# Kernel tuning notes

Measured on AMD Instinct MI355X. Metric: run time of the kernel, lower is better.

The kernel has to match this reference:

```python
import jax, jax.numpy as jnp
import numpy as np

B, N, T = 32, 128, 16          # batch, nb_nodes, total algorithm steps (1 no-hint + T-1 hinted)
FN, FE, FG, FH = 16, 8, 8, 16  # raw node/edge/graph/hint feature widths
H, DEC = 128, 64               # hidden_dim, decoder output width
MSG_STEPS = 3                  # msg_passing_steps
NEG = -1e9


def setup_inputs() -> dict:
    key = jax.random.key(0)
    ks = jax.random.split(key, 20)
    def nrm(k, shape, s=0.1):
        return jax.random.normal(k, shape, dtype=jnp.float32) * s
    return dict(
        node_inputs=nrm(ks[0], (B, N, FN), 1.0),
        edge_inputs=nrm(ks[1], (B, N, N, FE), 1.0),
        graph_inputs=nrm(ks[2], (B, FG), 1.0),
        hints_in=nrm(ks[3], (T - 1, B, N, FH), 1.0),
        adj=jax.random.randint(ks[4], (B, N, N), 0, 2).astype(jnp.int32),
        W_enc_n=nrm(ks[5], (FN, H)),
        W_enc_h=nrm(ks[6], (FH, H)),
        W_enc_e=nrm(ks[7], (FE, H)),
        W_enc_g=nrm(ks[8], (FG, H)),
        W_m1=nrm(ks[9], (2 * H, H)),
        W_m2=nrm(ks[10], (2 * H, H)),
        W_me=nrm(ks[11], (H, H)),
        W_mg=nrm(ks[12], (H, H)),
        W_o1=nrm(ks[13], (2 * H, H)),
        W_o2=nrm(ks[14], (H, H)),
        W_dec_n=nrm(ks[15], (H, DEC)),
        W_dec_e=nrm(ks[16], (H, DEC)),
    )


def reference(node_inputs, edge_inputs, graph_inputs, hints_in, adj,
              W_enc_n, W_enc_h, W_enc_e, W_enc_g,
              W_m1, W_m2, W_me, W_mg, W_o1, W_o2, W_dec_n, W_dec_e):
    adj_m = (adj > 0)[..., None]                      # [B,N,N,1] receiver i <- sender j
    # Encoder (edge/graph parts are step-invariant; hoisting is math-equivalent)
    edge_fts = edge_inputs @ W_enc_e                  # [B,N,N,H]
    graph_fts = graph_inputs @ W_enc_g                # [B,H]
    msg_e = edge_fts @ W_me                           # [B,N,N,H]
    msg_g = (graph_fts @ W_mg)[:, None, None, :]      # [B,1,1,H]
    base_node = node_inputs @ W_enc_n                 # [B,N,H]
    # Step 0 has no hint; steps 1..T-1 use hints_in[step-1]
    hints_all = jnp.concatenate(
        [jnp.zeros((1,) + hints_in.shape[1:], hints_in.dtype), hints_in], axis=0)

    def step(hidden, hint):
        node_fts = base_node + hint @ W_enc_h         # [B,N,H]
        edge_out = None
        for _ in range(MSG_STEPS):                    # PGN message passing
            z = jnp.concatenate([node_fts, hidden], axis=-1)   # [B,N,2H]
            msgs = jax.nn.relu((z @ W_m1)[:, :, None, :]
                               + (z @ W_m2)[:, None, :, :]
                               + msg_e + msg_g)       # [B,N,N,H]
            agg = jnp.where(adj_m, msgs, NEG).max(axis=2)      # max over senders j
            hidden = jax.nn.relu(z @ W_o1 + agg @ W_o2)        # [B,N,H]
            edge_out = msgs
        # Decoder: node head + masked-max-pooled edge head
        edge_agg = jnp.where(adj_m, edge_out, NEG).max(axis=2)
        out = hidden @ W_dec_n + edge_agg @ W_dec_e   # [B,N,DEC]
        return hidden, out

    hidden0 = jnp.zeros((node_inputs.shape[0], node_inputs.shape[1], H),
                        node_inputs.dtype)
    _, outs = jax.lax.scan(step, hidden0, hints_all)  # outs: [T,B,N,DEC]
    return outs
```

## Files before the change

kernel.cpp:

```cpp
#include <hip/hip_runtime.h>
#include <hip/hip_bf16.h>
#include <stdint.h>

#define BB 32
#define NN 128
#define TT 16
#define FN 16
#define FE 8
#define FG 8
#define FH 16
#define HH 128
#define DEC 64


__global__ __launch_bounds__(HH) void prep1(const float* __restrict__ node,
                                            const float* __restrict__ Wn,
                                            float* __restrict__ base_node,
                                            float* __restrict__ hid) {
    int row = blockIdx.x;
    int h = threadIdx.x;
    float acc = 0.f;
#pragma unroll
    for (int f = 0; f < FN; ++f)
        acc += node[row * FN + f] * Wn[f * HH + h];
    base_node[row * HH + h] = acc;
    hid[row * HH + h] = 0.f;
}

__global__ __launch_bounds__(HH) void prep2(const float* __restrict__ graph,
                                            const float* __restrict__ Wg,
                                            const float* __restrict__ Wmg,
                                            const float* __restrict__ Wee,
                                            const float* __restrict__ Wme,
                                            float* __restrict__ mg,
                                            float* __restrict__ We) {
    int h = threadIdx.x;
    if (blockIdx.x < BB) {
        int b = blockIdx.x;
        __shared__ float gf[HH];
        float acc = 0.f;
#pragma unroll
        for (int f = 0; f < FG; ++f) acc += graph[b * FG + f] * Wg[f * HH + h];
        gf[h] = acc;
        __syncthreads();
        float a2 = 0.f;
#pragma unroll 16
        for (int k = 0; k < HH; ++k) a2 += gf[k] * Wmg[k * HH + h];
        mg[b * HH + h] = a2;
    } else {
        int f = blockIdx.x - BB;
        float acc = 0.f;
#pragma unroll 16
        for (int k = 0; k < HH; ++k) acc += Wee[f * HH + k] * Wme[k * HH + h];
        We[f * HH + h] = acc;
    }
}

__device__ __forceinline__ uint32_t bf16rne(float v) {
    uint32_t b = __float_as_uint(v);
    return (b + 0x7fffu + ((b >> 16) & 1u)) >> 16;
}

__global__ __launch_bounds__(HH) void prep3(const float* __restrict__ edge,
                                            const int* __restrict__ adj,
                                            uint4* __restrict__ eg16,
                                            int* __restrict__ jl,
                                            int* __restrict__ cnt) {
    int bi = blockIdx.x;
    int j = threadIdx.x;
    __shared__ int w0cnt, totc, j0s;
    bool valid = adj[(size_t)bi * NN + j] > 0;
    unsigned long long mask = __ballot(valid);
    int lane = j & 63;
    int wave = j >> 6;
    int prefix = __popcll(mask & ((1ull << lane) - 1ull));
    int wcount = __popcll(mask);
    if (wave == 0 && lane == 0) w0cnt = wcount;
    __syncthreads();
    int base = (wave == 1) ? w0cnt : 0;
    if (wave == 1 && lane == 0) totc = w0cnt + wcount;
    int pos = base + prefix;
    if (valid && pos == 0) j0s = j;
    __syncthreads();
    int c = totc;
    int cpad = (c + 7) & ~7;
    if (j == 0) cnt[bi] = cpad;

    if (valid) {
        jl[bi * NN + pos] = j;
        const float* src = edge + ((size_t)bi * NN + j) * FE;
        uint4 r;
        r.x = bf16rne(src[0]) | (bf16rne(src[1]) << 16);
        r.y = bf16rne(src[2]) | (bf16rne(src[3]) << 16);
        r.z = bf16rne(src[4]) | (bf16rne(src[5]) << 16);
        r.w = bf16rne(src[6]) | (bf16rne(src[7]) << 16);
        eg16[(size_t)bi * NN + pos] = r;
    }
    if (c > 0 && j >= c && j < cpad) {
        int j0 = j0s;
        jl[bi * NN + j] = j0;
        const float* src = edge + ((size_t)bi * NN + j0) * FE;
        uint4 r;
        r.x = bf16rne(src[0]) | (bf16rne(src[1]) << 16);
        r.y = bf16rne(src[2]) | (bf16rne(src[3]) << 16);
        r.z = bf16rne(src[4]) | (bf16rne(src[5]) << 16);
        r.w = bf16rne(src[6]) | (bf16rne(src[7]) << 16);
        eg16[(size_t)bi * NN + j] = r;
    }
}

__global__ __launch_bounds__(256) void k0_nf(
    const float* __restrict__ base_node, const float* __restrict__ hints,
    const float* __restrict__ Wh,
    const float* __restrict__ Wm1, const float* __restrict__ Wm2,
    const float* __restrict__ Wo1, const float* __restrict__ mg,
    float* __restrict__ zpart) {
    __shared__ float zs[8][HH];
    const int lane = threadIdx.x & 127;
    const int half = threadIdx.x >> 7;
    const int bid = blockIdx.x;
    const int t = bid >> 9;
    const int bl = bid & 511;
    const int tile = (bl & 7) * 64 + (bl >> 3);
    const int row0 = tile * 8;

#pragma unroll
    for (int r = 0; r < 4; ++r) {
        int rr = half * 4 + r;
        int row = row0 + rr;
        float nf = base_node[row * HH + lane];
        if (t > 0) {
            const float* hr = hints + ((size_t)(t - 1) * BB * NN + row) * FH;
#pragma unroll
            for (int f = 0; f < FH; ++f) nf = fmaf(hr[f], Wh[f * HH + lane], nf);
        }
        zs[rr][lane] = nf;
    }
    __syncthreads();

    float acc[4][3];
#pragma unroll
    for (int r = 0; r < 4; ++r) { acc[r][0] = 0.f; acc[r][1] = 0.f; acc[r][2] = 0.f; }
    const int h4 = half * 4;

#pragma unroll 4
    for (int kk = 0; kk < 32; ++kk) {
        const int k0 = kk * 4;
        float4 z0 = *(const float4*)&zs[h4 + 0][k0];
        float4 z1 = *(const float4*)&zs[h4 + 1][k0];
        float4 z2 = *(const float4*)&zs[h4 + 2][k0];
        float4 z3 = *(const float4*)&zs[h4 + 3][k0];
#define K0U(COMP, KO)                                                   \
        {                                                               \
            const float w1 = Wm1[(k0 + KO) * HH + lane];                \
            const float w2 = Wm2[(k0 + KO) * HH + lane];                \
            const float w3 = Wo1[(k0 + KO) * HH + lane];                \
            acc[0][0] = fmaf(z0.COMP, w1, acc[0][0]);                   \
            acc[1][0] = fmaf(z1.COMP, w1, acc[1][0]);                   \
            acc[2][0] = fmaf(z2.COMP, w1, acc[2][0]);                   \
            acc[3][0] = fmaf(z3.COMP, w1, acc[3][0]);                   \
            acc[0][1] = fmaf(z0.COMP, w2, acc[0][1]);                   \
            acc[1][1] = fmaf(z1.COMP, w2, acc[1][1]);                   \
            acc[2][1] = fmaf(z2.COMP, w2, acc[2][1]);                   \
            acc[3][1] = fmaf(z3.COMP, w2, acc[3][1]);                   \
            acc[0][2] = fmaf(z0.COMP, w3, acc[0][2]);                   \
            acc[1][2] = fmaf(z1.COMP, w3, acc[1][2]);                   \
            acc[2][2] = fmaf(z2.COMP, w3, acc[2][2]);                   \
            acc[3][2] = fmaf(z3.COMP, w3, acc[3][2]);                   \
        }
        K0U(x, 0) K0U(y, 1) K0U(z, 2) K0U(w, 3)
#undef K0U
    }

    const int b = row0 >> 7;
    const float mgv = mg[b * HH + lane];
#pragma unroll
    for (int r = 0; r < 4; ++r) {
        const int row = row0 + h4 + r;
        const size_t o = ((size_t)t * 3 * 4096) * HH;
        zpart[o + ((size_t)0 * 4096 + row) * HH + lane] = acc[r][0] + mgv;
        zpart[o + ((size_t)1 * 4096 + row) * HH + lane] = acc[r][1];
        zpart[o + ((size_t)2 * 4096 + row) * HH + lane] = acc[r][2];
    }
}

__global__ __launch_bounds__(256) void k1_gemm(
    const float* __restrict__ hid,
    const float* __restrict__ Wm1, const float* __restrict__ Wm2,
    const float* __restrict__ Wo1, const float* __restrict__ zpart,
    float* __restrict__ m1p, float* __restrict__ m2, float* __restrict__ o1,
    int t) {
    __shared__ float zs[8][HH];
    const int lane = threadIdx.x & 127;
    const int half = threadIdx.x >> 7;
    const int bid = blockIdx.x;
    const int tile = (bid & 7) * 64 + (bid >> 3);
    const int row0 = tile * 8;

#pragma unroll
    for (int r = 0; r < 4; ++r) {
        int rr = half * 4 + r;
        zs[rr][lane] = hid[(row0 + rr) * HH + lane];
    }
    __syncthreads();

    float acc[4][3];
#pragma unroll
    for (int r = 0; r < 4; ++r) { acc[r][0] = 0.f; acc[r][1] = 0.f; acc[r][2] = 0.f; }
    const int h4 = half * 4;
    const float* __restrict__ W1 = Wm1 + HH * HH;
    const float* __restrict__ W2 = Wm2 + HH * HH;
    const float* __restrict__ W3 = Wo1 + HH * HH;

#pragma unroll 4
    for (int kk = 0; kk < 32; ++kk) {
        const int k0 = kk * 4;
        float4 z0 = *(const float4*)&zs[h4 + 0][k0];
        float4 z1 = *(const float4*)&zs[h4 + 1][k0];
        float4 z2 = *(const float4*)&zs[h4 + 2][k0];
        float4 z3 = *(const float4*)&zs[h4 + 3][k0];
#define K1U(COMP, KO)                                                   \
        {                                                               \
            const float w1 = W1[(k0 + KO) * HH + lane];                 \
            const float w2 = W2[(k0 + KO) * HH + lane];                 \
            const float w3 = W3[(k0 + KO) * HH + lane];                 \
            acc[0][0] = fmaf(z0.COMP, w1, acc[0][0]);                   \
            acc[1][0] = fmaf(z1.COMP, w1, acc[1][0]);                   \
            acc[2][0] = fmaf(z2.COMP, w1, acc[2][0]);                   \
            acc[3][0] = fmaf(z3.COMP, w1, acc[3][0]);                   \
            acc[0][1] = fmaf(z0.COMP, w2, acc[0][1]);                   \
            acc[1][1] = fmaf(z1.COMP, w2, acc[1][1]);                   \
            acc[2][1] = fmaf(z2.COMP, w2, acc[2][1]);                   \
            acc[3][1] = fmaf(z3.COMP, w2, acc[3][1]);                   \
            acc[0][2] = fmaf(z0.COMP, w3, acc[0][2]);                   \
            acc[1][2] = fmaf(z1.COMP, w3, acc[1][2]);                   \
            acc[2][2] = fmaf(z2.COMP, w3, acc[2][2]);                   \
            acc[3][2] = fmaf(z3.COMP, w3, acc[3][2]);                   \
        }
        K1U(x, 0) K1U(y, 1) K1U(z, 2) K1U(w, 3)
#undef K1U
    }

    const size_t zo = ((size_t)t * 3 * 4096) * HH;
#pragma unroll
    for (int r = 0; r < 4; ++r) {
        const int row = row0 + h4 + r;
        m1p[row * HH + lane] = acc[r][0] + zpart[zo + ((size_t)0 * 4096 + row) * HH + lane];
        m2[row * HH + lane]  = acc[r][1] + zpart[zo + ((size_t)1 * 4096 + row) * HH + lane];
        o1[row * HH + lane]  = acc[r][2] + zpart[zo + ((size_t)2 * 4096 + row) * HH + lane];
    }
}

__global__ __launch_bounds__(HH) void k2_max(
    const uint4* __restrict__ eg16, const int* __restrict__ jl,
    const int* __restrict__ cnt, const float* __restrict__ We,
    const float* __restrict__ m1p, const float* __restrict__ m2,
    const float* __restrict__ o1, const float* __restrict__ Wo2,
    const float* __restrict__ Wdn, const float* __restrict__ Wde,
    float* __restrict__ hid, float* __restrict__ out, int t, int last) {
    __shared__ float agg_lds[HH];
    __shared__ float hnew_lds[HH];
    const int h = threadIdx.x;
    const int bid = blockIdx.x;
    const int bi = (bid & 7) * 512 + (bid >> 3);
    const int b = bi >> 7;

    const float we0 = We[0 * HH + h], we1 = We[1 * HH + h];
    const float we2 = We[2 * HH + h], we3 = We[3 * HH + h];
    const float we4 = We[4 * HH + h], we5 = We[5 * HH + h];
    const float we6 = We[6 * HH + h], we7 = We[7 * HH + h];

    const uint4* __restrict__ egp = eg16 + (size_t)bi * NN;
    const int* __restrict__ jlb = jl + bi * NN;
    const float* __restrict__ m2b = m2 + (size_t)b * NN * HH;
    const int cp = cnt[bi];
    const float m1v = m1p[bi * HH + h];
    const float o1v = o1[bi * HH + h];

    float M = -3e38f;
    const int nch = cp >> 3;
    for (int ch = 0; ch < nch; ++ch) {
        const int k0 = ch * 8;
        uint4 raw[8];
        int jj[8];
        float mv[8];
#pragma unroll
        for (int s = 0; s < 8; ++s) raw[s] = egp[k0 + s];
#pragma unroll
        for (int s = 0; s < 8; ++s) jj[s] = jlb[k0 + s];
#pragma unroll
        for (int s = 0; s < 8; ++s) mv[s] = m2b[jj[s] * HH + h];
#pragma unroll
        for (int s = 0; s < 8; ++s) {
            uint32_t x = raw[s].x, y = raw[s].y, z = raw[s].z, w = raw[s].w;
            float e = __uint_as_float(x << 16) * we0;
            e = fmaf(__uint_as_float(x & 0xffff0000u), we1, e);
            e = fmaf(__uint_as_float(y << 16), we2, e);
            e = fmaf(__uint_as_float(y & 0xffff0000u), we3, e);
            e = fmaf(__uint_as_float(z << 16), we4, e);
            e = fmaf(__uint_as_float(z & 0xffff0000u), we5, e);
            e = fmaf(__uint_as_float(w << 16), we6, e);
            e = fmaf(__uint_as_float(w & 0xffff0000u), we7, e);
            M = fmaxf(M, e + mv[s]);
        }
    }
    float agg = (cp > 0) ? fmaxf(m1v + M, 0.f) : -1e9f;
    agg_lds[h] = agg;
    __syncthreads();

    float acc = o1v;
    const float4* a4 = (const float4*)agg_lds;
#pragma unroll 8
    for (int kk = 0; kk < 32; ++kk) {
        float4 a = a4[kk];
        acc = fmaf(a.x, Wo2[(kk * 4 + 0) * HH + h], acc);
        acc = fmaf(a.y, Wo2[(kk * 4 + 1) * HH + h], acc);
        acc = fmaf(a.z, Wo2[(kk * 4 + 2) * HH + h], acc);
        acc = fmaf(a.w, Wo2[(kk * 4 + 3) * HH + h], acc);
    }
    float hv = fmaxf(acc, 0.f);
    hid[bi * HH + h] = hv;

    if (last) {
        hnew_lds[h] = hv;
        __syncthreads();
        if (h < DEC) {
            float a = 0.f, e2 = 0.f;
            const float4* h4p = (const float4*)hnew_lds;
#pragma unroll 8
            for (int kk = 0; kk < 32; ++kk) {
                float4 hv4 = h4p[kk];
                float4 av4 = a4[kk];
                a = fmaf(hv4.x, Wdn[(kk * 4 + 0) * DEC + h], a);
                a = fmaf(hv4.y, Wdn[(kk * 4 + 1) * DEC + h], a);
                a = fmaf(hv4.z, Wdn[(kk * 4 + 2) * DEC + h], a);
                a = fmaf(hv4.w, Wdn[(kk * 4 + 3) * DEC + h], a);
                e2 = fmaf(av4.x, Wde[(kk * 4 + 0) * DEC + h], e2);
                e2 = fmaf(av4.y, Wde[(kk * 4 + 1) * DEC + h], e2);
                e2 = fmaf(av4.z, Wde[(kk * 4 + 2) * DEC + h], e2);
                e2 = fmaf(av4.w, Wde[(kk * 4 + 3) * DEC + h], e2);
            }
            out[(((size_t)t * BB + b) * NN + (bi & 127)) * DEC + h] = a + e2;
        }
    }
}

extern "C" void kernel_launch(void* const* d_in, const int* in_sizes, int n_in,
                              void* d_out, int out_size, void* d_ws, size_t ws_size,
                              hipStream_t stream) {
    const float* node = (const float*)d_in[0];
    const float* edge = (const float*)d_in[1];
    const float* graph = (const float*)d_in[2];
    const float* hints = (const float*)d_in[3];
    const int* adj = (const int*)d_in[4];
    const float* Wn = (const float*)d_in[5];
    const float* Wh = (const float*)d_in[6];
    const float* Wee = (const float*)d_in[7];
    const float* Wg = (const float*)d_in[8];
    const float* Wm1 = (const float*)d_in[9];
    const float* Wm2 = (const float*)d_in[10];
    const float* Wme = (const float*)d_in[11];
    const float* Wmg = (const float*)d_in[12];
    const float* Wo1 = (const float*)d_in[13];
    const float* Wo2 = (const float*)d_in[14];
    const float* Wdn = (const float*)d_in[15];
    const float* Wde = (const float*)d_in[16];

    float* ws = (float*)d_ws;
    float* base_node = ws;
    float* We = ws + 524288;
    float* mg = ws + 525312;
    float* m1p = ws + 529408;
    float* m2 = ws + 1053696;
    float* o1 = ws + 1577984;
    float* hid = ws + 2102272;
    uint4* eg16 = (uint4*)(ws + 2626560);
    int* jl = (int*)(ws + 4723712);
    int* cnt = (int*)(ws + 5248000);
    float* zpart = ws + 5252096;
    float* out = (float*)d_out;

    prep1<<<BB * NN, HH, 0, stream>>>(node, Wn, base_node, hid);
    prep2<<<BB + FE, HH, 0, stream>>>(graph, Wg, Wmg, Wee, Wme, mg, We);
    prep3<<<BB * NN, HH, 0, stream>>>(edge, adj, eg16, jl, cnt);
    k0_nf<<<8192, 256, 0, stream>>>(base_node, hints, Wh, Wm1, Wm2, Wo1, mg,
                                    zpart);

    for (int t = 0; t < TT; ++t) {
        for (int ms = 0; ms < 3; ++ms) {
            k1_gemm<<<512, 256, 0, stream>>>(hid, Wm1, Wm2, Wo1, zpart,
                                             m1p, m2, o1, t);
            k2_max<<<BB * NN, HH, 0, stream>>>(eg16, jl, cnt, We, m1p, m2, o1,
                                               Wo2, Wdn, Wde, hid, out, t,
                                               ms == 2 ? 1 : 0);
        }
    }
}
```

Measured before the change: 2.058 ms.

## Fuse message max-aggregation with next-iteration GEMM into a single kernel

Merges the separate GEMM and max-aggregation kernels into one 1024-thread kernel per 8-row tile. Each launch stages the batch's m2 projection into LDS, computes the masked max, the Wo2 update and optionally the decoder, then immediately computes the next iteration's m1/m2/o1 from the new hidden state in LDS. Outputs go to ping-pong buffers, so launches drop from 96 to 48 and the hidden-state round trip through global memory disappears. The cost is 64KB+ of LDS per block, which limits occupancy, and only 256 of 1024 threads do the next-step GEMM.

```diff
diff --git a/kernel.cpp b/kernel.cpp
--- a/kernel.cpp
+++ b/kernel.cpp
@@ -15,8 +15,7 @@
 
 __global__ __launch_bounds__(HH) void prep1(const float* __restrict__ node,
                                             const float* __restrict__ Wn,
-                                            float* __restrict__ base_node,
-                                            float* __restrict__ hid) {
+                                            float* __restrict__ base_node) {
     int row = blockIdx.x;
     int h = threadIdx.x;
     float acc = 0.f;
@@ -24,7 +23,6 @@
     for (int f = 0; f < FN; ++f)
         acc += node[row * FN + f] * Wn[f * HH + h];
     base_node[row * HH + h] = acc;
-    hid[row * HH + h] = 0.f;
 }
 
 __global__ __launch_bounds__(HH) void prep2(const float* __restrict__ graph,
@@ -184,114 +182,64 @@
     }
 }
 
-__global__ __launch_bounds__(256) void k1_gemm(
-    const float* __restrict__ hid,
+__global__ __launch_bounds__(1024, 8) void k12(
+    const uint4* __restrict__ eg16, const int* __restrict__ jl,
+    const int* __restrict__ cnt, const float* __restrict__ We,
+    const float* __restrict__ m1c, const float* __restrict__ m2c,
+    const float* __restrict__ o1c,
     const float* __restrict__ Wm1, const float* __restrict__ Wm2,
-    const float* __restrict__ Wo1, const float* __restrict__ zpart,
-    float* __restrict__ m1p, float* __restrict__ m2, float* __restrict__ o1,
-    int t) {
-    __shared__ float zs[8][HH];
-    const int lane = threadIdx.x & 127;
-    const int half = threadIdx.x >> 7;
+    const float* __restrict__ Wo1, const float* __restrict__ Wo2,
+    const float* __restrict__ Wdn, const float* __restrict__ Wde,
+    const float* __restrict__ zp,
+    float* __restrict__ m1n, float* __restrict__ m2n, float* __restrict__ o1n,
+    float* __restrict__ out, int t, int last, int do_next) {
+    __shared__ float m2_lds[NN][HH];
+    __shared__ float agg_lds[8][HH];
+    __shared__ float hv_lds[8][HH];
+    const int tid = threadIdx.x;
     const int bid = blockIdx.x;
     const int tile = (bid & 7) * 64 + (bid >> 3);
-    const int row0 = tile * 8;
-
-#pragma unroll
-    for (int r = 0; r < 4; ++r) {
-        int rr = half * 4 + r;
-        zs[rr][lane] = hid[(row0 + rr) * HH + lane];
-    }
-    __syncthreads();
-
-    float acc[4][3];
-#pragma unroll
-    for (int r = 0; r < 4; ++r) { acc[r][0] = 0.f; acc[r][1] = 0.f; acc[r][2] = 0.f; }
-    const int h4 = half * 4;
-    const float* __restrict__ W1 = Wm1 + HH * HH;
-    const float* __restrict__ W2 = Wm2 + HH * HH;
-    const float* __restrict__ W3 = Wo1 + HH * HH;
-
-#pragma unroll 4
-    for (int kk = 0; kk < 32; ++kk) {
-        const int k0 = kk * 4;
-        float4 z0 = *(const float4*)&zs[h4 + 0][k0];
-        float4 z1 = *(const float4*)&zs[h4 + 1][k0];
-        float4 z2 = *(const float4*)&zs[h4 + 2][k0];
-        float4 z3 = *(const float4*)&zs[h4 + 3][k0];
-#define K1U(COMP, KO)                                                   \
-        {                                                               \
-            const float w1 = W1[(k0 + KO) * HH + lane];                 \
-            const float w2 = W2[(k0 + KO) * HH + lane];                 \
-            const float w3 = W3[(k0 + KO) * HH + lane];                 \
-            acc[0][0] = fmaf(z0.COMP, w1, acc[0][0]);                   \
-            acc[1][0] = fmaf(z1.COMP, w1, acc[1][0]);                   \
-            acc[2][0] = fmaf(z2.COMP, w1, acc[2][0]);                   \
-            acc[3][0] = fmaf(z3.COMP, w1, acc[3][0]);                   \
-            acc[0][1] = fmaf(z0.COMP, w2, acc[0][1]);                   \
-            acc[1][1] = fmaf(z1.COMP, w2, acc[1][1]);                   \
-            acc[2][1] = fmaf(z2.COMP, w2, acc[2][1]);                   \
-            acc[3][1] = fmaf(z3.COMP, w2, acc[3][1]);                   \
-            acc[0][2] = fmaf(z0.COMP, w3, acc[0][2]);                   \
-            acc[1][2] = fmaf(z1.COMP, w3, acc[1][2]);                   \
-            acc[2][2] = fmaf(z2.COMP, w3, acc[2][2]);                   \
-            acc[3][2] = fmaf(z3.COMP, w3, acc[3][2]);                   \
-        }
-        K1U(x, 0) K1U(y, 1) K1U(z, 2) K1U(w, 3)
-#undef K1U
-    }
-
-    const size_t zo = ((size_t)t * 3 * 4096) * HH;
-#pragma unroll
-    for (int r = 0; r < 4; ++r) {
-        const int row = row0 + h4 + r;
-        m1p[row * HH + lane] = acc[r][0] + zpart[zo + ((size_t)0 * 4096 + row) * HH + lane];
-        m2[row * HH + lane]  = acc[r][1] + zpart[zo + ((size_t)1 * 4096 + row) * HH + lane];
-        o1[row * HH + lane]  = acc[r][2] + zpart[zo + ((size_t)2 * 4096 + row) * HH + lane];
-    }
-}
-
-__global__ __launch_bounds__(HH) void k2_max(
-    const uint4* __restrict__ eg16, const int* __restrict__ jl,
-    const int* __restrict__ cnt, const float* __restrict__ We,
-    const float* __restrict__ m1p, const float* __restrict__ m2,
-    const float* __restrict__ o1, const float* __restrict__ Wo2,
-    const float* __restrict__ Wdn, const float* __restrict__ Wde,
-    float* __restrict__ hid, float* __restrict__ out, int t, int last) {
-    __shared__ float agg_lds[HH];
-    __shared__ float hnew_lds[HH];
-    const int h = threadIdx.x;
-    const int bid = blockIdx.x;
-    const int bi = (bid & 7) * 512 + (bid >> 3);
-    const int b = bi >> 7;
+    const int b = tile >> 4;
+    const int ig = tile & 15;
+    const int bi0 = b * NN + ig * 8;
+
+    {
+        const float4* src = (const float4*)(m2c + (size_t)b * NN * HH);
+        float4* dst = (float4*)&m2_lds[0][0];
+#pragma unroll
+        for (int u = 0; u < 4; ++u) dst[u * 1024 + tid] = src[u * 1024 + tid];
+    }
+
+    const int il = tid >> 7;
+    const int h = tid & 127;
+    const int bi = bi0 + il;
 
     const float we0 = We[0 * HH + h], we1 = We[1 * HH + h];
     const float we2 = We[2 * HH + h], we3 = We[3 * HH + h];
     const float we4 = We[4 * HH + h], we5 = We[5 * HH + h];
     const float we6 = We[6 * HH + h], we7 = We[7 * HH + h];
-
+    const int cp = cnt[bi];
+    const float m1v = m1c[bi * HH + h];
+    const float o1v = o1c[bi * HH + h];
     const uint4* __restrict__ egp = eg16 + (size_t)bi * NN;
     const int* __restrict__ jlb = jl + bi * NN;
-    const float* __restrict__ m2b = m2 + (size_t)b * NN * HH;
-    const int cp = cnt[bi];
-    const float m1v = m1p[bi * HH + h];
-    const float o1v = o1[bi * HH + h];
+    __syncthreads();
 
     float M = -3e38f;
-    const int nch = cp >> 3;
+    const int nch = cp >> 2;
     for (int ch = 0; ch < nch; ++ch) {
-        const int k0 = ch * 8;
-        uint4 raw[8];
-        int jj[8];
-        float mv[8];
-#pragma unroll
-        for (int s = 0; s < 8; ++s) raw[s] = egp[k0 + s];
-#pragma unroll
-        for (int s = 0; s < 8; ++s) jj[s] = jlb[k0 + s];
-#pragma unroll
-        for (int s = 0; s < 8; ++s) mv[s] = m2b[jj[s] * HH + h];
-#pragma unroll
-        for (int s = 0; s < 8; ++s) {
+        const int k0 = ch * 4;
+        uint4 raw[4];
+        int jj[4];
+        float mv[4];
+#pragma unroll
+        for (int s = 0; s < 4; ++s) raw[s] = egp[k0 + s];
+#pragma unroll
+        for (int s = 0; s < 4; ++s) jj[s] = jlb[k0 + s];
+#pragma unroll
+        for (int s = 0; s < 4; ++s) mv[s] = m2_lds[jj[s]][h];
+#pragma unroll
+        for (int s = 0; s < 4; ++s) {
             uint32_t x = raw[s].x, y = raw[s].y, z = raw[s].z, w = raw[s].w;
             float e = __uint_as_float(x << 16) * we0;
             e = fmaf(__uint_as_float(x & 0xffff0000u), we1, e);
@@ -305,11 +253,11 @@
         }
     }
     float agg = (cp > 0) ? fmaxf(m1v + M, 0.f) : -1e9f;
-    agg_lds[h] = agg;
+    agg_lds[il][h] = agg;
     __syncthreads();
 
     float acc = o1v;
-    const float4* a4 = (const float4*)agg_lds;
+    const float4* a4 = (const float4*)&agg_lds[il][0];
 #pragma unroll 8
     for (int kk = 0; kk < 32; ++kk) {
         float4 a = a4[kk];
@@ -318,29 +266,81 @@
         acc = fmaf(a.z, Wo2[(kk * 4 + 2) * HH + h], acc);
         acc = fmaf(a.w, Wo2[(kk * 4 + 3) * HH + h], acc);
     }
-    float hv = fmaxf(acc, 0.f);
-    hid[bi * HH + h] = hv;
-
-    if (last) {
-        hnew_lds[h] = hv;
-        __syncthreads();
-        if (h < DEC) {
-            float a = 0.f, e2 = 0.f;
-            const float4* h4p = (const float4*)hnew_lds;
+    hv_lds[il][h] = fmaxf(acc, 0.f);
+    __syncthreads();
+
+    if (last && tid >= 512) {
+        const int dl = (tid - 512) >> 6;
+        const int hh = (tid - 512) & 63;
+        float a = 0.f, e2 = 0.f;
+        const float4* h4p = (const float4*)&hv_lds[dl][0];
+        const float4* ag4 = (const float4*)&agg_lds[dl][0];
 #pragma unroll 8
-            for (int kk = 0; kk < 32; ++kk) {
-                float4 hv4 = h4p[kk];
-                float4 av4 = a4[kk];
-                a = fmaf(hv4.x, Wdn[(kk * 4 + 0) * DEC + h], a);
-                a = fmaf(hv4.y, Wdn[(kk * 4 + 1) * DEC + h], a);
-                a = fmaf(hv4.z, Wdn[(kk * 4 + 2) * DEC + h], a);
-                a = fmaf(hv4.w, Wdn[(kk * 4 + 3) * DEC + h], a);
-                e2 = fmaf(av4.x, Wde[(kk * 4 + 0) * DEC + h], e2);
-                e2 = fmaf(av4.y, Wde[(kk * 4 + 1) * DEC + h], e2);
-                e2 = fmaf(av4.z, Wde[(kk * 4 + 2) * DEC + h], e2);
-                e2 = fmaf(av4.w, Wde[(kk * 4 + 3) * DEC + h], e2);
+        for (int kk = 0; kk < 32; ++kk) {
+            float4 hv4 = h4p[kk];
+            float4 av4 = ag4[kk];
+            a = fmaf(hv4.x, Wdn[(kk * 4 + 0) * DEC + hh], a);
+            a = fmaf(hv4.y, Wdn[(kk * 4 + 1) * DEC + hh], a);
+            a = fmaf(hv4.z, Wdn[(kk * 4 + 2) * DEC + hh], a);
+            a = fmaf(hv4.w, Wdn[(kk * 4 + 3) * DEC + hh], a);
+            e2 = fmaf(av4.x, Wde[(kk * 4 + 0) * DEC + hh], e2);
+            e2 = fmaf(av4.y, Wde[(kk * 4 + 1) * DEC + hh], e2);
+            e2 = fmaf(av4.z, Wde[(kk * 4 + 2) * DEC + hh], e2);
+            e2 = fmaf(av4.w, Wde[(kk * 4 + 3) * DEC + hh], e2);
+        }
+        out[(((size_t)t * BB + b) * NN + ig * 8 + dl) * DEC + hh] = a + e2;
+    }
+
+    if (do_next && tid < 256) {
+        const int lane = tid & 127;
+        const int half = tid >> 7;
+        const int h4 = half * 4;
+        const float* __restrict__ W1 = Wm1 + HH * HH;
+        const float* __restrict__ W2 = Wm2 + HH * HH;
+        const float* __restrict__ W3 = Wo1 + HH * HH;
+
+        float acc2[4][3];
+#pragma unroll
+        for (int r = 0; r < 4; ++r) {
+            acc2[r][0] = 0.f; acc2[r][1] = 0.f; acc2[r][2] = 0.f;
+        }
+#pragma unroll 4
+        for (int kk = 0; kk < 32; ++kk) {
+            const int k0 = kk * 4;
+            float4 z0 = *(const float4*)&hv_lds[h4 + 0][k0];
+            float4 z1 = *(const float4*)&hv_lds[h4 + 1][k0];
+            float4 z2 = *(const float4*)&hv_lds[h4 + 2][k0];
+            float4 z3 = *(const float4*)&hv_lds[h4 + 3][k0];
+#define K1U(COMP, KO)                                                   \
+            {                                                           \
+                const float w1 = W1[(k0 + KO) * HH + lane];             \
+                const float w2 = W2[(k0 + KO) * HH + lane];             \
+                const float w3 = W3[(k0 + KO) * HH + lane];             \
+                acc2[0][0] = fmaf(z0.COMP, w1, acc2[0][0]);             \
+                acc2[1][0] = fmaf(z1.COMP, w1, acc2[1][0]);             \
+                acc2[2][0] = fmaf(z2.COMP, w1, acc2[2][0]);             \
+                acc2[3][0] = fmaf(z3.COMP, w1, acc2[3][0]);             \
+                acc2[0][1] = fmaf(z0.COMP, w2, acc2[0][1]);             \
+                acc2[1][1] = fmaf(z1.COMP, w2, acc2[1][1]);             \
+                acc2[2][1] = fmaf(z2.COMP, w2, acc2[2][1]);             \
+                acc2[3][1] = fmaf(z3.COMP, w2, acc2[3][1]);             \
+                acc2[0][2] = fmaf(z0.COMP, w3, acc2[0][2]);             \
+                acc2[1][2] = fmaf(z1.COMP, w3, acc2[1][2]);             \
+                acc2[2][2] = fmaf(z2.COMP, w3, acc2[2][2]);             \
+                acc2[3][2] = fmaf(z3.COMP, w3, acc2[3][2]);             \
             }
-            out[(((size_t)t * BB + b) * NN + (bi & 127)) * DEC + h] = a + e2;
+            K1U(x, 0) K1U(y, 1) K1U(z, 2) K1U(w, 3)
+#undef K1U
+        }
+#pragma unroll
+        for (int r = 0; r < 4; ++r) {
+            const int row = bi0 + h4 + r;
+            m1n[(size_t)row * HH + lane] =
+                acc2[r][0] + zp[((size_t)0 * 4096 + row) * HH + lane];
+            m2n[(size_t)row * HH + lane] =
+                acc2[r][1] + zp[((size_t)1 * 4096 + row) * HH + lane];
+            o1n[(size_t)row * HH + lane] =
+                acc2[r][2] + zp[((size_t)2 * 4096 + row) * HH + lane];
         }
     }
 }
@@ -370,29 +370,46 @@
     float* base_node = ws;
     float* We = ws + 524288;
     float* mg = ws + 525312;
-    float* m1p = ws + 529408;
-    float* m2 = ws + 1053696;
-    float* o1 = ws + 1577984;
-    float* hid = ws + 2102272;
-    uint4* eg16 = (uint4*)(ws + 2626560);
-    int* jl = (int*)(ws + 4723712);
-    int* cnt = (int*)(ws + 5248000);
-    float* zpart = ws + 5252096;
+    uint4* eg16 = (uint4*)(ws + 529408);
+    int* jl = (int*)(ws + 2626560);
+    int* cnt = (int*)(ws + 3150848);
+    float* zpart = ws + 3154944;
+    float* bufA = ws + 28320768;
+    float* bufB = ws + 29893632;
     float* out = (float*)d_out;
 
-    prep1<<<BB * NN, HH, 0, stream>>>(node, Wn, base_node, hid);
+    const size_t MS = (size_t)4096 * HH;
+
+    prep1<<<BB * NN, HH, 0, stream>>>(node, Wn, base_node);
     prep2<<<BB + FE, HH, 0, stream>>>(graph, Wg, Wmg, Wee, Wme, mg, We);
     prep3<<<BB * NN, HH, 0, stream>>>(edge, adj, eg16, jl, cnt);
     k0_nf<<<8192, 256, 0, stream>>>(base_node, hints, Wh, Wm1, Wm2, Wo1, mg,
                                     zpart);
 
-    for (int t = 0; t < TT; ++t) {
-        for (int ms = 0; ms < 3; ++ms) {
-            k1_gemm<<<512, 256, 0, stream>>>(hid, Wm1, Wm2, Wo1, zpart,
-                                             m1p, m2, o1, t);
-            k2_max<<<BB * NN, HH, 0, stream>>>(eg16, jl, cnt, We, m1p, m2, o1,
-                                               Wo2, Wdn, Wde, hid, out, t,
-                                               ms == 2 ? 1 : 0);
-        }
-    }
-}
+    for (int r = 0; r < 48; ++r) {
+        const int t = r / 3;
+        const int ms = r % 3;
+        const int last = (ms == 2) ? 1 : 0;
+        const int tn = t + last;
+        const int do_next = (r < 47) ? 1 : 0;
+
+        const float *m1c, *m2c, *o1c;
+        if (r == 0) {
+            m1c = zpart;
+            m2c = zpart + MS;
+            o1c = zpart + 2 * MS;
+        } else {
+            float* cb = ((r - 1) & 1) ? bufB : bufA;
+            m1c = cb; m2c = cb + MS; o1c = cb + 2 * MS;
+        }
+        float* nb = (r & 1) ? bufB : bufA;
+        float* m1n = nb;
+        float* m2n = nb + MS;
+        float* o1n = nb + 2 * MS;
+        const float* zp = zpart + (size_t)(do_next ? tn : 0) * 3 * MS;
+
+        k12<<<512, 1024, 0, stream>>>(eg16, jl, cnt, We, m1c, m2c, o1c,
+                                      Wm1, Wm2, Wo1, Wo2, Wdn, Wde, zp,
+                                      m1n, m2n, o1n, out, t, last, do_next);
+    }
+}
```

Result: slower. 2.521 ms (+22.5%).

## Fold hint encoder into precomputed weights, skip first hidden GEMM, widen k1 blocks

Applied to the files above, without the earlier changes.

Precomputes Wh·W for the three first-half weight slices and a base_node·W term once, so each k1_gemm adds the hint contribution through a 16-wide FMA instead of reading a 16-step precomputed zpart buffer. The first message step (hidden is zero) skips k1_gemm and feeds baseW straight to k2_max, and prep1 no longer zeroes hid. k1 blocks go from 256 to 512 threads with 2 rows per thread group to raise occupancy. This trades a large per-timestep zpart workspace and its writes for slightly more arithmetic inside k1.

```diff
diff --git a/kernel.cpp b/kernel.cpp
--- a/kernel.cpp
+++ b/kernel.cpp
@@ -15,8 +15,7 @@
 
 __global__ __launch_bounds__(HH) void prep1(const float* __restrict__ node,
                                             const float* __restrict__ Wn,
-                                            float* __restrict__ base_node,
-                                            float* __restrict__ hid) {
+                                            float* __restrict__ base_node) {
     int row = blockIdx.x;
     int h = threadIdx.x;
     float acc = 0.f;
@@ -24,7 +23,6 @@
     for (int f = 0; f < FN; ++f)
         acc += node[row * FN + f] * Wn[f * HH + h];
     base_node[row * HH + h] = acc;
-    hid[row * HH + h] = 0.f;
 }
 
 __global__ __launch_bounds__(HH) void prep2(const float* __restrict__ graph,
@@ -109,116 +107,107 @@
     }
 }
 
-__global__ __launch_bounds__(256) void k0_nf(
-    const float* __restrict__ base_node, const float* __restrict__ hints,
-    const float* __restrict__ Wh,
+__global__ __launch_bounds__(HH) void prepW(
+    const float* __restrict__ Wh, const float* __restrict__ Wm1,
+    const float* __restrict__ Wm2, const float* __restrict__ Wo1,
+    float* __restrict__ WhW) {
+    const int h = threadIdx.x;
+    const int m = blockIdx.x >> 4;
+    const int f = blockIdx.x & 15;
+    const float* __restrict__ W = (m == 0) ? Wm1 : (m == 1) ? Wm2 : Wo1;
+    float acc = 0.f;
+#pragma unroll 16
+    for (int k = 0; k < HH; ++k)
+        acc = fmaf(Wh[f * HH + k], W[k * HH + h], acc);
+    WhW[(m * FH + f) * HH + h] = acc;
+}
+
+__global__ __launch_bounds__(512, 4) void prepB(
+    const float* __restrict__ base_node,
     const float* __restrict__ Wm1, const float* __restrict__ Wm2,
     const float* __restrict__ Wo1, const float* __restrict__ mg,
-    float* __restrict__ zpart) {
+    float* __restrict__ baseW) {
     __shared__ float zs[8][HH];
-    const int lane = threadIdx.x & 127;
-    const int half = threadIdx.x >> 7;
+    const int tid = threadIdx.x;
+    const int lane = tid & 127;
+    const int grp = tid >> 7;
     const int bid = blockIdx.x;
-    const int t = bid >> 9;
-    const int bl = bid & 511;
-    const int tile = (bl & 7) * 64 + (bl >> 3);
+    const int tile = (bid & 7) * 64 + (bid >> 3);
     const int row0 = tile * 8;
-
-#pragma unroll
-    for (int r = 0; r < 4; ++r) {
-        int rr = half * 4 + r;
-        int row = row0 + rr;
-        float nf = base_node[row * HH + lane];
-        if (t > 0) {
-            const float* hr = hints + ((size_t)(t - 1) * BB * NN + row) * FH;
-#pragma unroll
-            for (int f = 0; f < FH; ++f) nf = fmaf(hr[f], Wh[f * HH + lane], nf);
-        }
-        zs[rr][lane] = nf;
-    }
+    const int rg0 = grp * 2, rg1 = rg0 + 1;
+
+    zs[rg0][lane] = base_node[(size_t)(row0 + rg0) * HH + lane];
+    zs[rg1][lane] = base_node[(size_t)(row0 + rg1) * HH + lane];
     __syncthreads();
 
-    float acc[4][3];
-#pragma unroll
-    for (int r = 0; r < 4; ++r) { acc[r][0] = 0.f; acc[r][1] = 0.f; acc[r][2] = 0.f; }
-    const int h4 = half * 4;
+    float acc[2][3];
+#pragma unroll
+    for (int e = 0; e < 2; ++e) { acc[e][0] = 0.f; acc[e][1] = 0.f; acc[e][2] = 0.f; }
 
 #pragma unroll 4
     for (int kk = 0; kk < 32; ++kk) {
         const int k0 = kk * 4;
-        float4 z0 = *(const float4*)&zs[h4 + 0][k0];
-        float4 z1 = *(const float4*)&zs[h4 + 1][k0];
-        float4 z2 = *(const float4*)&zs[h4 + 2][k0];
-        float4 z3 = *(const float4*)&zs[h4 + 3][k0];
-#define K0U(COMP, KO)                                                   \
+        float4 z0 = *(const float4*)&zs[rg0][k0];
+        float4 z1 = *(const float4*)&zs[rg1][k0];
+#define PBU(COMP, KO)                                                   \
         {                                                               \
             const float w1 = Wm1[(k0 + KO) * HH + lane];                \
             const float w2 = Wm2[(k0 + KO) * HH + lane];                \
             const float w3 = Wo1[(k0 + KO) * HH + lane];                \
             acc[0][0] = fmaf(z0.COMP, w1, acc[0][0]);                   \
             acc[1][0] = fmaf(z1.COMP, w1, acc[1][0]);                   \
-            acc[2][0] = fmaf(z2.COMP, w1, acc[2][0]);                   \
-            acc[3][0] = fmaf(z3.COMP, w1, acc[3][0]);                   \
             acc[0][1] = fmaf(z0.COMP, w2, acc[0][1]);                   \
             acc[1][1] = fmaf(z1.COMP, w2, acc[1][1]);                   \
-            acc[2][1] = fmaf(z2.COMP, w2, acc[2][1]);                   \
-            acc[3][1] = fmaf(z3.COMP, w2, acc[3][1]);                   \
             acc[0][2] = fmaf(z0.COMP, w3, acc[0][2]);                   \
             acc[1][2] = fmaf(z1.COMP, w3, acc[1][2]);                   \
-            acc[2][2] = fmaf(z2.COMP, w3, acc[2][2]);                   \
-            acc[3][2] = fmaf(z3.COMP, w3, acc[3][2]);                   \
-        }
-        K0U(x, 0) K0U(y, 1) K0U(z, 2) K0U(w, 3)
-#undef K0U
-    }
-
-    const int b = row0 >> 7;
-    const float mgv = mg[b * HH + lane];
-#pragma unroll
-    for (int r = 0; r < 4; ++r) {
-        const int row = row0 + h4 + r;
-        const size_t o = ((size_t)t * 3 * 4096) * HH;
-        zpart[o + ((size_t)0 * 4096 + row) * HH + lane] = acc[r][0] + mgv;
-        zpart[o + ((size_t)1 * 4096 + row) * HH + lane] = acc[r][1];
-        zpart[o + ((size_t)2 * 4096 + row) * HH + lane] = acc[r][2];
-    }
-}
-
-__global__ __launch_bounds__(256) void k1_gemm(
+        }
+        PBU(x, 0) PBU(y, 1) PBU(z, 2) PBU(w, 3)
+#undef PBU
+    }
+
+#pragma unroll
+    for (int e = 0; e < 2; ++e) {
+        const int row = row0 + grp * 2 + e;
+        const float mgv = mg[(row >> 7) * HH + lane];
+        baseW[((size_t)0 * 4096 + row) * HH + lane] = acc[e][0] + mgv;
+        baseW[((size_t)1 * 4096 + row) * HH + lane] = acc[e][1];
+        baseW[((size_t)2 * 4096 + row) * HH + lane] = acc[e][2];
+    }
+}
+
+__global__ __launch_bounds__(512, 4) void k1_gemm(
     const float* __restrict__ hid,
     const float* __restrict__ Wm1, const float* __restrict__ Wm2,
-    const float* __restrict__ Wo1, const float* __restrict__ zpart,
-    float* __restrict__ m1p, float* __restrict__ m2, float* __restrict__ o1,
+    const float* __restrict__ Wo1, const float* __restrict__ baseW,
+    const float* __restrict__ WhW, const float* __restrict__ hints,
+    float* __restrict__ m1n, float* __restrict__ m2n, float* __restrict__ o1n,
     int t) {
     __shared__ float zs[8][HH];
-    const int lane = threadIdx.x & 127;
-    const int half = threadIdx.x >> 7;
+    const int tid = threadIdx.x;
+    const int lane = tid & 127;
+    const int grp = tid >> 7;
     const int bid = blockIdx.x;
     const int tile = (bid & 7) * 64 + (bid >> 3);
     const int row0 = tile * 8;
-
-#pragma unroll
-    for (int r = 0; r < 4; ++r) {
-        int rr = half * 4 + r;
-        zs[rr][lane] = hid[(row0 + rr) * HH + lane];
-    }
+    const int rg0 = grp * 2, rg1 = rg0 + 1;
+
+    zs[rg0][lane] = hid[(size_t)(row0 + rg0) * HH + lane];
+    zs[rg1][lane] = hid[(size_t)(row0 + rg1) * HH + lane];
     __syncthreads();
 
-    float acc[4][3];
-#pragma unroll
-    for (int r = 0; r < 4; ++r) { acc[r][0] = 0.f; acc[r][1] = 0.f; acc[r][2] = 0.f; }
-    const int h4 = half * 4;
     const float* __restrict__ W1 = Wm1 + HH * HH;
     const float* __restrict__ W2 = Wm2 + HH * HH;
     const float* __restrict__ W3 = Wo1 + HH * HH;
 
+    float acc[2][3];
+#pragma unroll
+    for (int e = 0; e < 2; ++e) { acc[e][0] = 0.f; acc[e][1] = 0.f; acc[e][2] = 0.f; }
+
 #pragma unroll 4
     for (int kk = 0; kk < 32; ++kk) {
         const int k0 = kk * 4;
-        float4 z0 = *(const float4*)&zs[h4 + 0][k0];
-        float4 z1 = *(const float4*)&zs[h4 + 1][k0];
-        float4 z2 = *(const float4*)&zs[h4 + 2][k0];
-        float4 z3 = *(const float4*)&zs[h4 + 3][k0];
+        float4 z0 = *(const float4*)&zs[rg0][k0];
+        float4 z1 = *(const float4*)&zs[rg1][k0];
 #define K1U(COMP, KO)                                                   \
         {                                                               \
             const float w1 = W1[(k0 + KO) * HH + lane];                 \
@@ -226,28 +215,35 @@
             const float w3 = W3[(k0 + KO) * HH + lane];                 \
             acc[0][0] = fmaf(z0.COMP, w1, acc[0][0]);                   \
             acc[1][0] = fmaf(z1.COMP, w1, acc[1][0]);                   \
-            acc[2][0] = fmaf(z2.COMP, w1, acc[2][0]);                   \
-            acc[3][0] = fmaf(z3.COMP, w1, acc[3][0]);                   \
             acc[0][1] = fmaf(z0.COMP, w2, acc[0][1]);                   \
             acc[1][1] = fmaf(z1.COMP, w2, acc[1][1]);                   \
-            acc[2][1] = fmaf(z2.COMP, w2, acc[2][1]);                   \
-            acc[3][1] = fmaf(z3.COMP, w2, acc[3][1]);                   \
             acc[0][2] = fmaf(z0.COMP, w3, acc[0][2]);                   \
             acc[1][2] = fmaf(z1.COMP, w3, acc[1][2]);                   \
-            acc[2][2] = fmaf(z2.COMP, w3, acc[2][2]);                   \
-            acc[3][2] = fmaf(z3.COMP, w3, acc[3][2]);                   \
         }
         K1U(x, 0) K1U(y, 1) K1U(z, 2) K1U(w, 3)
 #undef K1U
     }
 
-    const size_t zo = ((size_t)t * 3 * 4096) * HH;
-#pragma unroll
-    for (int r = 0; r < 4; ++r) {
-        const int row = row0 + h4 + r;
-        m1p[row * HH + lane] = acc[r][0] + zpart[zo + ((size_t)0 * 4096 + row) * HH + lane];
-        m2[row * HH + lane]  = acc[r][1] + zpart[zo + ((size_t)1 * 4096 + row) * HH + lane];
-        o1[row * HH + lane]  = acc[r][2] + zpart[zo + ((size_t)2 * 4096 + row) * HH + lane];
+#pragma unroll
+    for (int e = 0; e < 2; ++e) {
+        const int row = row0 + grp * 2 + e;
+        float s0 = baseW[((size_t)0 * 4096 + row) * HH + lane];
+        float s1 = baseW[((size_t)1 * 4096 + row) * HH + lane];
+        float s2 = baseW[((size_t)2 * 4096 + row) * HH + lane];
+        if (t > 0) {
+            const float* __restrict__ hr =
+                hints + ((size_t)(t - 1) * BB * NN + row) * FH;
+#pragma unroll
+            for (int f = 0; f < FH; ++f) {
+                const float hf = hr[f];
+                s0 = fmaf(hf, WhW[(0 * FH + f) * HH + lane], s0);
+                s1 = fmaf(hf, WhW[(1 * FH + f) * HH + lane], s1);
+                s2 = fmaf(hf, WhW[(2 * FH + f) * HH + lane], s2);
+            }
+        }
+        m1n[(size_t)row * HH + lane] = acc[e][0] + s0;
+        m2n[(size_t)row * HH + lane] = acc[e][1] + s1;
+        o1n[(size_t)row * HH + lane] = acc[e][2] + s2;
     }
 }
 
@@ -274,8 +270,8 @@
     const int* __restrict__ jlb = jl + bi * NN;
     const float* __restrict__ m2b = m2 + (size_t)b * NN * HH;
     const int cp = cnt[bi];
-    const float m1v = m1p[bi * HH + h];
-    const float o1v = o1[bi * HH + h];
+    const float m1v = m1p[(size_t)bi * HH + h];
+    const float o1v = o1[(size_t)bi * HH + h];
 
     float M = -3e38f;
     const int nch = cp >> 3;
@@ -319,7 +315,7 @@
         acc = fmaf(a.w, Wo2[(kk * 4 + 3) * HH + h], acc);
     }
     float hv = fmaxf(acc, 0.f);
-    hid[bi * HH + h] = hv;
+    hid[(size_t)bi * HH + h] = hv;
 
     if (last) {
         hnew_lds[h] = hv;
@@ -370,29 +366,43 @@
     float* base_node = ws;
     float* We = ws + 524288;
     float* mg = ws + 525312;
-    float* m1p = ws + 529408;
-    float* m2 = ws + 1053696;
-    float* o1 = ws + 1577984;
-    float* hid = ws + 2102272;
-    uint4* eg16 = (uint4*)(ws + 2626560);
-    int* jl = (int*)(ws + 4723712);
-    int* cnt = (int*)(ws + 5248000);
-    float* zpart = ws + 5252096;
+    uint4* eg16 = (uint4*)(ws + 529408);
+    int* jl = (int*)(ws + 2626560);
+    int* cnt = (int*)(ws + 3150848);
+    float* WhW = ws + 3154944;
+    float* baseW = ws + 3161088;
+    float* m1p = ws + 4733952;
+    float* m2 = ws + 5258240;
+    float* o1 = ws + 5782528;
+    float* hid = ws + 6306816;
     float* out = (float*)d_out;
 
-    prep1<<<BB * NN, HH, 0, stream>>>(node, Wn, base_node, hid);
+    const size_t MS = (size_t)4096 * HH;
+
+    prep1<<<BB * NN, HH, 0, stream>>>(node, Wn, base_node);
     prep2<<<BB + FE, HH, 0, stream>>>(graph, Wg, Wmg, Wee, Wme, mg, We);
     prep3<<<BB * NN, HH, 0, stream>>>(edge, adj, eg16, jl, cnt);
-    k0_nf<<<8192, 256, 0, stream>>>(base_node, hints, Wh, Wm1, Wm2, Wo1, mg,
-                                    zpart);
-
-    for (int t = 0; t < TT; ++t) {
-        for (int ms = 0; ms < 3; ++ms) {
-            k1_gemm<<<512, 256, 0, stream>>>(hid, Wm1, Wm2, Wo1, zpart,
-                                             m1p, m2, o1, t);
-            k2_max<<<BB * NN, HH, 0, stream>>>(eg16, jl, cnt, We, m1p, m2, o1,
-                                               Wo2, Wdn, Wde, hid, out, t,
-                                               ms == 2 ? 1 : 0);
-        }
-    }
-}
+    prepW<<<48, HH, 0, stream>>>(Wh, Wm1, Wm2, Wo1, WhW);
+    prepB<<<512, 512, 0, stream>>>(base_node, Wm1, Wm2, Wo1, mg, baseW);
+
+    for (int r = 0; r < 48; ++r) {
+        const int t = r / 3;
+        const int ms = r % 3;
+        const int last = (ms == 2) ? 1 : 0;
+
+        const float *m1c, *m2c, *o1c;
+        if (r == 0) {
+            m1c = baseW;
+            m2c = baseW + MS;
+            o1c = baseW + 2 * MS;
+        } else {
+            k1_gemm<<<512, 512, 0, stream>>>(hid, Wm1, Wm2, Wo1, baseW, WhW,
+                                             hints, m1p, m2, o1, t);
+            m1c = m1p;
+            m2c = m2;
+            o1c = o1;
+        }
+        k2_max<<<BB * NN, HH, 0, stream>>>(eg16, jl, cnt, We, m1c, m2c, o1c,
+                                           Wo2, Wdn, Wde, hid, out, t, last);
+    }
+}
```

Measured after the change: 2.168 ms. +5.4%, slower.
